# Performance work log

Hardware: AMD Instinct MI355X
Metric: run time of the kernel (lower is better)

Reference implementation:

```python
import jax, jax.numpy as jnp
import numpy as np

RADIUS = 0.15   # group_args['radius']
NSAMPLE = 32    # group_args['nsample']
EPS = 1e-5      # BatchNorm eps


def ball_query(p, radius, k):
    # p: [B,N,3]; returns neighbor indices [B,N,K] (first K points within radius,
    # padded with the first hit -- PointNet++ ball-query semantics; self is always a hit)
    N = p.shape[1]
    d2 = jnp.sum((p[:, :, None, :] - p[:, None, :, :]) ** 2, axis=-1)  # [B,N,N]
    idx = jnp.where(d2 < radius * radius,
                    jnp.arange(N, dtype=jnp.int32)[None, None, :], N)
    idx = jnp.sort(idx, axis=-1)[..., :k]
    return jnp.where(idx == N, idx[..., :1], idx)


def conv_bn_relu(x, W, gamma, beta, mean, var):
    # 1x1 conv2d (pointwise over [N,K]) + eval-mode BN2d + ReLU
    x = jnp.einsum('oc,bcnk->bonk', W, x)
    scale = (gamma / jnp.sqrt(var + EPS))[None, :, None, None]
    shift = (beta - mean * gamma / jnp.sqrt(var + EPS))[None, :, None, None]
    return jax.nn.relu(x * scale + shift)


def setup_inputs() -> dict:
    key = jax.random.key(0)
    ks = jax.random.split(key, 4)
    B, N, C = 2, 8192, 64
    C1, C2 = 128, 128
    Cin = C + 3  # CHANNEL_MAP['dp_fj']
    return {
        'p': jax.random.uniform(ks[0], (B, N, 3), jnp.float32),
        'f': jax.random.normal(ks[1], (B, C, N), jnp.float32),
        'W1': jax.random.normal(ks[2], (C1, Cin), jnp.float32) / np.float32(np.sqrt(Cin)),
        'gamma1': jnp.ones((C1,), jnp.float32),
        'beta1': jnp.zeros((C1,), jnp.float32),
        'mean1': jnp.zeros((C1,), jnp.float32),
        'var1': jnp.ones((C1,), jnp.float32),
        'W2': jax.random.normal(ks[3], (C2, C1), jnp.float32) / np.float32(np.sqrt(C1)),
        'gamma2': jnp.ones((C2,), jnp.float32),
        'beta2': jnp.zeros((C2,), jnp.float32),
        'mean2': jnp.zeros((C2,), jnp.float32),
        'var2': jnp.ones((C2,), jnp.float32),
    }


def reference(p, f, W1, gamma1, beta1, mean1, var1, W2, gamma2, beta2, mean2, var2):
    # p: [B,N,3], f: [B,C,N]
    idx = ball_query(p, RADIUS, NSAMPLE)                                   # [B,N,K]
    gp = jnp.take_along_axis(p[:, None, :, :], idx[:, :, :, None], axis=2)  # [B,N,K,3]
    dp = jnp.transpose(gp - p[:, :, None, :], (0, 3, 1, 2))                 # [B,3,N,K]
    fj = jnp.take_along_axis(f[:, :, None, :], idx[:, None, :, :], axis=3)  # [B,C,N,K]
    x = jnp.concatenate([dp, fj], axis=1)                                   # dp_fj: [B,3+C,N,K]
    x = conv_bn_relu(x, W1, gamma1, beta1, mean1, var1)
    x = conv_bn_relu(x, W2, gamma2, beta2, mean2, var2)
    return jnp.max(x, axis=-1)                                              # [B,C2,N]
```

## Files before the change

kernel.cpp:

```cpp
#include <hip/hip_runtime.h>
#include <math.h>

#define NSAMPLE 32
constexpr int B_ = 2, N_ = 8192, C_ = 64, C1_ = 128, C2_ = 128, CIN_ = 67;
constexpr int KP = 96;
constexpr int XPAD = 104;
constexpr int HPAD = 136;
constexpr float BQ_R2 = 0.15f * 0.15f;
constexpr float EPS_ = 1e-5f;

typedef __attribute__((ext_vector_type(8))) short bf16x8;
typedef __attribute__((ext_vector_type(4))) short short4v;
typedef __attribute__((ext_vector_type(4))) float f32x4;

__device__ __forceinline__ short f2bf(float x) {
    union { float f; unsigned u; } v; v.f = x;
    return (short)((v.u + 0x7FFFu + ((v.u >> 16) & 1u)) >> 16);
}

constexpr int TBLK = (B_ * N_) / 256;
constexpr int QBLK0 = TBLK + 1;

__global__ __launch_bounds__(256) void prep_query_kernel(
    const float* __restrict__ p, const float* __restrict__ f,
    short* __restrict__ fT, int* __restrict__ idx,
    const float* __restrict__ W1,
    const float* __restrict__ g1, const float* __restrict__ b1,
    const float* __restrict__ m1, const float* __restrict__ v1,
    const float* __restrict__ W2,
    const float* __restrict__ g2, const float* __restrict__ b2,
    const float* __restrict__ m2, const float* __restrict__ v2,
    short* __restrict__ W1p, short* __restrict__ W2p, float* __restrict__ bn)
{
    int blk = blockIdx.x;
    if (blk < TBLK) {
        int g = blk * 256 + threadIdx.x;
        int b = g >> 13, n = g & (N_ - 1);
        const float* fb = f + (size_t)b * C_ * N_ + n;
        short* row = fT + (size_t)g * C_;
        #pragma unroll
        for (int c0 = 0; c0 < C_; c0 += 8) {
            bf16x8 v;
            #pragma unroll
            for (int c = 0; c < 8; ++c) v[c] = f2bf(fb[(size_t)(c0 + c) * N_]);
            *(bf16x8*)&row[c0] = v;
        }
    } else if (blk == TBLK) {
        if (threadIdx.x >= 128) return;
        int t = threadIdx.x;
        short* r1 = W1p + t * KP;
        #pragma unroll
        for (int k = 0; k < 3; ++k) r1[k] = f2bf(W1[t * CIN_ + k]);
        #pragma unroll
        for (int k = 3; k < 8; ++k) r1[k] = 0;
        for (int c = 0; c < 64; ++c) r1[8 + c] = f2bf(W1[t * CIN_ + 3 + c]);
        #pragma unroll
        for (int k = 72; k < KP; ++k) r1[k] = 0;
        short* r2 = W2p + t * C1_;
        for (int c = 0; c < C1_; ++c) r2[c] = f2bf(W2[t * C1_ + c]);
        float s1 = g1[t] * rsqrtf(v1[t] + EPS_);
        bn[t] = s1;            bn[128 + t] = b1[t] - m1[t] * s1;
        float s2 = g2[t] * rsqrtf(v2[t] + EPS_);
        bn[256 + t] = s2;      bn[384 + t] = b2[t] - m2[t] * s2;
    } else {
        int wid = (blk - QBLK0) * 4 + (threadIdx.x >> 6);
        int lane = threadIdx.x & 63;
        int b = wid >> 13, n = wid & (N_ - 1);
        const float* pb = p + (size_t)b * N_ * 3;
        float qx = pb[3 * n], qy = pb[3 * n + 1], qz = pb[3 * n + 2];
        int* out = idx + (size_t)wid * NSAMPLE;
        int cnt = 0, first = -1;
        for (int j0 = 0; j0 < N_; j0 += 256) {
            int jb = j0 + 4 * lane;
            const float* q = pb + 3 * jb;
            f32x4 u0 = *(const f32x4*)(q);
            f32x4 u1 = *(const f32x4*)(q + 4);
            f32x4 u2 = *(const f32x4*)(q + 8);
            float x0 = u0[0], y0 = u0[1], z0 = u0[2];
            float x1 = u0[3], y1 = u1[0], z1 = u1[1];
            float x2 = u1[2], y2 = u1[3], z2 = u2[0];
            float x3 = u2[1], y3 = u2[2], z3 = u2[3];
            float dx, dy, dz, d2;
            dx = __fadd_rn(x0, -qx); dy = __fadd_rn(y0, -qy); dz = __fadd_rn(z0, -qz);
            d2 = __fadd_rn(__fadd_rn(__fmul_rn(dx, dx), __fmul_rn(dy, dy)), __fmul_rn(dz, dz));
            bool h0 = d2 < BQ_R2;
            dx = __fadd_rn(x1, -qx); dy = __fadd_rn(y1, -qy); dz = __fadd_rn(z1, -qz);
            d2 = __fadd_rn(__fadd_rn(__fmul_rn(dx, dx), __fmul_rn(dy, dy)), __fmul_rn(dz, dz));
            bool h1 = d2 < BQ_R2;
            dx = __fadd_rn(x2, -qx); dy = __fadd_rn(y2, -qy); dz = __fadd_rn(z2, -qz);
            d2 = __fadd_rn(__fadd_rn(__fmul_rn(dx, dx), __fmul_rn(dy, dy)), __fmul_rn(dz, dz));
            bool h2 = d2 < BQ_R2;
            dx = __fadd_rn(x3, -qx); dy = __fadd_rn(y3, -qy); dz = __fadd_rn(z3, -qz);
            d2 = __fadd_rn(__fadd_rn(__fmul_rn(dx, dx), __fmul_rn(dy, dy)), __fmul_rn(dz, dz));
            bool h3 = d2 < BQ_R2;
            unsigned long long m0 = __ballot(h0), m1 = __ballot(h1);
            unsigned long long m2 = __ballot(h2), m3 = __ballot(h3);
            unsigned long long below = (1ull << lane) - 1ull;
            int pos = cnt + __popcll(m0 & below) + __popcll(m1 & below)
                          + __popcll(m2 & below) + __popcll(m3 & below);
            if (h0) { if (pos < NSAMPLE) out[pos] = jb;     ++pos; }
            if (h1) { if (pos < NSAMPLE) out[pos] = jb + 1; ++pos; }
            if (h2) { if (pos < NSAMPLE) out[pos] = jb + 2; ++pos; }
            if (h3) { if (pos < NSAMPLE) out[pos] = jb + 3; ++pos; }
            if (first < 0) {
                int fj = 0x7fffffff;
                if (m0) fj = min(fj, 4 * (__ffsll((long long)m0) - 1));
                if (m1) fj = min(fj, 4 * (__ffsll((long long)m1) - 1) + 1);
                if (m2) fj = min(fj, 4 * (__ffsll((long long)m2) - 1) + 2);
                if (m3) fj = min(fj, 4 * (__ffsll((long long)m3) - 1) + 3);
                if (fj != 0x7fffffff) first = j0 + fj;
            }
            cnt += __popcll(m0) + __popcll(m1) + __popcll(m2) + __popcll(m3);
            if (cnt >= NSAMPLE) break;
        }
        for (int k2 = cnt + lane; k2 < NSAMPLE; k2 += 64) out[k2] = first;
    }
}

__global__ __launch_bounds__(256) void fused_mfma_kernel(
    const float* __restrict__ p, const int* __restrict__ idx,
    const short* __restrict__ fT, const short* __restrict__ W1p,
    const short* __restrict__ W2p, const float* __restrict__ bn,
    float* __restrict__ out)
{
    __shared__ short smem[128 * HPAD];
    __shared__ float sBN[4][128];
    __shared__ int sidx[128];

    int tid = threadIdx.x;
    int bk = blockIdx.x;
    bk = (bk & 7) * 512 + (bk >> 3);
    int b = bk >> 11;
    int n0 = (bk & 2047) * 4;
    int lane = tid & 63, w = tid >> 6;
    int lr = lane & 15, lq = lane >> 4;

    if (tid < 128) {
        sBN[0][tid] = bn[tid];       sBN[1][tid] = bn[128 + tid];
        sBN[2][tid] = bn[256 + tid]; sBN[3][tid] = bn[384 + tid];
        sidx[tid] = idx[((size_t)((b << 13) + n0)) * NSAMPLE + tid];
    }
    __syncthreads();

    const float* pb = p + (size_t)b * N_ * 3;
    #pragma unroll
    for (int pass = 0; pass < 4; ++pass) {
        int col = pass * 32 + (tid >> 3);
        int part = tid & 7;
        int j = sidx[col];
        *(bf16x8*)&smem[col * XPAD + 8 + part * 8] =
            *(const bf16x8*)&fT[((size_t)(b << 13) + j) * C_ + part * 8];
        if (part == 0) {
            int n = n0 + (col >> 5);
            bf16x8 v = {0, 0, 0, 0, 0, 0, 0, 0};
            v[0] = f2bf(__fadd_rn(pb[3 * j],     -pb[3 * n]));
            v[1] = f2bf(__fadd_rn(pb[3 * j + 1], -pb[3 * n + 1]));
            v[2] = f2bf(__fadd_rn(pb[3 * j + 2], -pb[3 * n + 2]));
            *(bf16x8*)&smem[col * XPAD] = v;
        } else if (part <= 3) {
            bf16x8 z = {0, 0, 0, 0, 0, 0, 0, 0};
            *(bf16x8*)&smem[col * XPAD + 72 + (part - 1) * 8] = z;
        }
    }
    __syncthreads();

    int wr = (w & 1) * 64;
    int wc = (w >> 1) * 64;

    f32x4 acc[4][4];
    #pragma unroll
    for (int m = 0; m < 4; ++m)
        #pragma unroll
        for (int nt = 0; nt < 4; ++nt) acc[m][nt] = (f32x4){0.f, 0.f, 0.f, 0.f};
    #pragma unroll
    for (int ks = 0; ks < 3; ++ks) {
        bf16x8 a[4];
        #pragma unroll
        for (int m = 0; m < 4; ++m)
            a[m] = *(const bf16x8*)&W1p[(wr + m * 16 + lr) * KP + ks * 32 + lq * 8];
        #pragma unroll
        for (int nt = 0; nt < 4; ++nt) {
            bf16x8 bf = *(const bf16x8*)&smem[(wc + nt * 16 + lr) * XPAD + ks * 32 + lq * 8];
            #pragma unroll
            for (int m = 0; m < 4; ++m)
                acc[m][nt] = __builtin_amdgcn_mfma_f32_16x16x32_bf16(a[m], bf, acc[m][nt], 0, 0, 0);
        }
    }
    __syncthreads();

    #pragma unroll
    for (int m = 0; m < 4; ++m) {
        int rb = wr + m * 16 + lq * 4;
        float s0 = sBN[0][rb], s1 = sBN[0][rb + 1], s2 = sBN[0][rb + 2], s3 = sBN[0][rb + 3];
        float h0 = sBN[1][rb], h1 = sBN[1][rb + 1], h2 = sBN[1][rb + 2], h3 = sBN[1][rb + 3];
        #pragma unroll
        for (int nt = 0; nt < 4; ++nt) {
            int col = wc + nt * 16 + lr;
            short4v hv;
            hv[0] = f2bf(fmaxf(fmaf(acc[m][nt][0], s0, h0), 0.f));
            hv[1] = f2bf(fmaxf(fmaf(acc[m][nt][1], s1, h1), 0.f));
            hv[2] = f2bf(fmaxf(fmaf(acc[m][nt][2], s2, h2), 0.f));
            hv[3] = f2bf(fmaxf(fmaf(acc[m][nt][3], s3, h3), 0.f));
            *(short4v*)&smem[col * HPAD + rb] = hv;
        }
    }
    __syncthreads();

    f32x4 acc2[4][4];
    #pragma unroll
    for (int m = 0; m < 4; ++m)
        #pragma unroll
        for (int nt = 0; nt < 4; ++nt) acc2[m][nt] = (f32x4){0.f, 0.f, 0.f, 0.f};
    #pragma unroll
    for (int ks = 0; ks < 4; ++ks) {
        bf16x8 a[4];
        #pragma unroll
        for (int m = 0; m < 4; ++m)
            a[m] = *(const bf16x8*)&W2p[(wr + m * 16 + lr) * C1_ + ks * 32 + lq * 8];
        #pragma unroll
        for (int nt = 0; nt < 4; ++nt) {
            bf16x8 bf = *(const bf16x8*)&smem[(wc + nt * 16 + lr) * HPAD + ks * 32 + lq * 8];
            #pragma unroll
            for (int m = 0; m < 4; ++m)
                acc2[m][nt] = __builtin_amdgcn_mfma_f32_16x16x32_bf16(a[m], bf, acc2[m][nt], 0, 0, 0);
        }
    }

    #pragma unroll
    for (int m = 0; m < 4; ++m) {
        int rb = wr + m * 16 + lq * 4;
        float s0 = sBN[2][rb], s1 = sBN[2][rb + 1], s2 = sBN[2][rb + 2], s3 = sBN[2][rb + 3];
        float h0 = sBN[3][rb], h1 = sBN[3][rb + 1], h2 = sBN[3][rb + 2], h3 = sBN[3][rb + 3];
        #pragma unroll
        for (int lp = 0; lp < 2; ++lp) {
            int n = n0 + (w >> 1) * 2 + lp;
            float v0 = fmaxf(fmaf(acc2[m][2 * lp][0], s0, h0), fmaf(acc2[m][2 * lp + 1][0], s0, h0));
            float v1 = fmaxf(fmaf(acc2[m][2 * lp][1], s1, h1), fmaf(acc2[m][2 * lp + 1][1], s1, h1));
            float v2 = fmaxf(fmaf(acc2[m][2 * lp][2], s2, h2), fmaf(acc2[m][2 * lp + 1][2], s2, h2));
            float v3 = fmaxf(fmaf(acc2[m][2 * lp][3], s3, h3), fmaf(acc2[m][2 * lp + 1][3], s3, h3));
            #pragma unroll
            for (int st = 1; st <= 8; st <<= 1) {
                v0 = fmaxf(v0, __shfl_xor(v0, st, 64));
                v1 = fmaxf(v1, __shfl_xor(v1, st, 64));
                v2 = fmaxf(v2, __shfl_xor(v2, st, 64));
                v3 = fmaxf(v3, __shfl_xor(v3, st, 64));
            }
            if (lr == 0) {
                out[((size_t)(b * C2_ + rb))     * N_ + n] = fmaxf(v0, 0.f);
                out[((size_t)(b * C2_ + rb + 1)) * N_ + n] = fmaxf(v1, 0.f);
                out[((size_t)(b * C2_ + rb + 2)) * N_ + n] = fmaxf(v2, 0.f);
                out[((size_t)(b * C2_ + rb + 3)) * N_ + n] = fmaxf(v3, 0.f);
            }
        }
    }
}

extern "C" void kernel_launch(void* const* d_in, const int* in_sizes, int n_in,
                              void* d_out, int out_size, void* d_ws, size_t ws_size,
                              hipStream_t stream) {
    const float* p   = (const float*)d_in[0];
    const float* f   = (const float*)d_in[1];
    const float* W1  = (const float*)d_in[2];
    const float* g1  = (const float*)d_in[3];
    const float* bb1 = (const float*)d_in[4];
    const float* m1  = (const float*)d_in[5];
    const float* v1  = (const float*)d_in[6];
    const float* W2  = (const float*)d_in[7];
    const float* g2  = (const float*)d_in[8];
    const float* bb2 = (const float*)d_in[9];
    const float* m2  = (const float*)d_in[10];
    const float* v2  = (const float*)d_in[11];
    float* out = (float*)d_out;

    char* ws = (char*)d_ws;
    int*   idxbuf = (int*)ws;
    short* fT  = (short*)(ws + (2 << 20));
    short* W1p = (short*)(ws + (4 << 20));
    short* W2p = (short*)(ws + (4 << 20) + 0x6000);
    float* bnv = (float*)(ws + (4 << 20) + 0xE000);

    prep_query_kernel<<<QBLK0 + (B_ * N_) / 4, 256, 0, stream>>>(
        p, f, fT, idxbuf, W1, g1, bb1, m1, v1, W2, g2, bb2, m2, v2,
        W1p, W2p, bnv);
    fused_mfma_kernel<<<(B_ * N_) / 4, 256, 0, stream>>>(
        p, idxbuf, fT, W1p, W2p, bnv, out);
}
```

Baseline: 181.3 us.

## Precompute relative offsets in ball query and swizzle LDS tiles in fused MLP

The ball-query stage now writes bf16 relative offsets (dp) alongside neighbor indices, so the fused kernel no longer gathers point coordinates. The fused kernel drops row padding in LDS in favor of an XOR swizzle, preloads W1 fragments into registers, and reads BN parameters straight from global memory. Packed bf16 conversion instructions replace manual rounding, and the query loop prefetches the next chunk of points. This trades extra workspace writes and register pressure for fewer scattered global loads and LDS bank conflicts.

After: 205.0 us. 13.1% more time.

```diff
diff --git a/kernel.cpp b/kernel.cpp
--- a/kernel.cpp
+++ b/kernel.cpp
@@ -4,26 +4,29 @@
 #define NSAMPLE 32
 constexpr int B_ = 2, N_ = 8192, C_ = 64, C1_ = 128, C2_ = 128, CIN_ = 67;
 constexpr int KP = 96;
-constexpr int XPAD = 104;
-constexpr int HPAD = 136;
 constexpr float BQ_R2 = 0.15f * 0.15f;
 constexpr float EPS_ = 1e-5f;
 
 typedef __attribute__((ext_vector_type(8))) short bf16x8;
-typedef __attribute__((ext_vector_type(4))) short short4v;
 typedef __attribute__((ext_vector_type(4))) float f32x4;
+typedef unsigned long long ull;
 
 __device__ __forceinline__ short f2bf(float x) {
     union { float f; unsigned u; } v; v.f = x;
     return (short)((v.u + 0x7FFFu + ((v.u >> 16) & 1u)) >> 16);
 }
+__device__ __forceinline__ unsigned cvt_pk_bf16(float a, float b) {
+    unsigned r;
+    asm("v_cvt_pk_bf16_f32 %0, %1, %2" : "=v"(r) : "v"(a), "v"(b));
+    return r;
+}
 
 constexpr int TBLK = (B_ * N_) / 256;
 constexpr int QBLK0 = TBLK + 1;
 
 __global__ __launch_bounds__(256) void prep_query_kernel(
     const float* __restrict__ p, const float* __restrict__ f,
-    short* __restrict__ fT, int* __restrict__ idx,
+    short* __restrict__ fT, int* __restrict__ idx, short* __restrict__ dpq,
     const float* __restrict__ W1,
     const float* __restrict__ g1, const float* __restrict__ b1,
     const float* __restrict__ m1, const float* __restrict__ v1,
@@ -40,10 +43,14 @@
         short* row = fT + (size_t)g * C_;
         #pragma unroll
         for (int c0 = 0; c0 < C_; c0 += 8) {
-            bf16x8 v;
-            #pragma unroll
-            for (int c = 0; c < 8; ++c) v[c] = f2bf(fb[(size_t)(c0 + c) * N_]);
-            *(bf16x8*)&row[c0] = v;
+            float t0 = fb[(size_t)(c0 + 0) * N_], t1 = fb[(size_t)(c0 + 1) * N_];
+            float t2 = fb[(size_t)(c0 + 2) * N_], t3 = fb[(size_t)(c0 + 3) * N_];
+            float t4 = fb[(size_t)(c0 + 4) * N_], t5 = fb[(size_t)(c0 + 5) * N_];
+            float t6 = fb[(size_t)(c0 + 6) * N_], t7 = fb[(size_t)(c0 + 7) * N_];
+            union { bf16x8 v; unsigned u[4]; } uu;
+            uu.u[0] = cvt_pk_bf16(t0, t1); uu.u[1] = cvt_pk_bf16(t2, t3);
+            uu.u[2] = cvt_pk_bf16(t4, t5); uu.u[3] = cvt_pk_bf16(t6, t7);
+            *(bf16x8*)&row[c0] = uu.v;
         }
     } else if (blk == TBLK) {
         if (threadIdx.x >= 128) return;
@@ -69,39 +76,49 @@
         const float* pb = p + (size_t)b * N_ * 3;
         float qx = pb[3 * n], qy = pb[3 * n + 1], qz = pb[3 * n + 2];
         int* out = idx + (size_t)wid * NSAMPLE;
+        short* dq = dpq + (size_t)wid * NSAMPLE * 4;
         int cnt = 0, first = -1;
+        const float* q0 = pb + 12 * lane;
+        f32x4 u0 = *(const f32x4*)(q0);
+        f32x4 u1 = *(const f32x4*)(q0 + 4);
+        f32x4 u2 = *(const f32x4*)(q0 + 8);
         for (int j0 = 0; j0 < N_; j0 += 256) {
+            int jn = (j0 + 256 < N_) ? j0 + 256 : 0;
+            const float* qn = pb + 3 * (jn + 4 * lane);
+            f32x4 w0 = *(const f32x4*)(qn);
+            f32x4 w1 = *(const f32x4*)(qn + 4);
+            f32x4 w2 = *(const f32x4*)(qn + 8);
             int jb = j0 + 4 * lane;
-            const float* q = pb + 3 * jb;
-            f32x4 u0 = *(const f32x4*)(q);
-            f32x4 u1 = *(const f32x4*)(q + 4);
-            f32x4 u2 = *(const f32x4*)(q + 8);
             float x0 = u0[0], y0 = u0[1], z0 = u0[2];
             float x1 = u0[3], y1 = u1[0], z1 = u1[1];
             float x2 = u1[2], y2 = u1[3], z2 = u2[0];
             float x3 = u2[1], y3 = u2[2], z3 = u2[3];
-            float dx, dy, dz, d2;
-            dx = __fadd_rn(x0, -qx); dy = __fadd_rn(y0, -qy); dz = __fadd_rn(z0, -qz);
-            d2 = __fadd_rn(__fadd_rn(__fmul_rn(dx, dx), __fmul_rn(dy, dy)), __fmul_rn(dz, dz));
-            bool h0 = d2 < BQ_R2;
-            dx = __fadd_rn(x1, -qx); dy = __fadd_rn(y1, -qy); dz = __fadd_rn(z1, -qz);
-            d2 = __fadd_rn(__fadd_rn(__fmul_rn(dx, dx), __fmul_rn(dy, dy)), __fmul_rn(dz, dz));
-            bool h1 = d2 < BQ_R2;
-            dx = __fadd_rn(x2, -qx); dy = __fadd_rn(y2, -qy); dz = __fadd_rn(z2, -qz);
-            d2 = __fadd_rn(__fadd_rn(__fmul_rn(dx, dx), __fmul_rn(dy, dy)), __fmul_rn(dz, dz));
-            bool h2 = d2 < BQ_R2;
-            dx = __fadd_rn(x3, -qx); dy = __fadd_rn(y3, -qy); dz = __fadd_rn(z3, -qz);
-            d2 = __fadd_rn(__fadd_rn(__fmul_rn(dx, dx), __fmul_rn(dy, dy)), __fmul_rn(dz, dz));
-            bool h3 = d2 < BQ_R2;
-            unsigned long long m0 = __ballot(h0), m1 = __ballot(h1);
-            unsigned long long m2 = __ballot(h2), m3 = __ballot(h3);
-            unsigned long long below = (1ull << lane) - 1ull;
+            float ax0 = __fadd_rn(x0, -qx), ay0 = __fadd_rn(y0, -qy), az0 = __fadd_rn(z0, -qz);
+            float ax1 = __fadd_rn(x1, -qx), ay1 = __fadd_rn(y1, -qy), az1 = __fadd_rn(z1, -qz);
+            float ax2 = __fadd_rn(x2, -qx), ay2 = __fadd_rn(y2, -qy), az2 = __fadd_rn(z2, -qz);
+            float ax3 = __fadd_rn(x3, -qx), ay3 = __fadd_rn(y3, -qy), az3 = __fadd_rn(z3, -qz);
+            float d20 = __fadd_rn(__fadd_rn(__fmul_rn(ax0, ax0), __fmul_rn(ay0, ay0)), __fmul_rn(az0, az0));
+            float d21 = __fadd_rn(__fadd_rn(__fmul_rn(ax1, ax1), __fmul_rn(ay1, ay1)), __fmul_rn(az1, az1));
+            float d22 = __fadd_rn(__fadd_rn(__fmul_rn(ax2, ax2), __fmul_rn(ay2, ay2)), __fmul_rn(az2, az2));
+            float d23 = __fadd_rn(__fadd_rn(__fmul_rn(ax3, ax3), __fmul_rn(ay3, ay3)), __fmul_rn(az3, az3));
+            bool h0 = d20 < BQ_R2, h1 = d21 < BQ_R2, h2 = d22 < BQ_R2, h3 = d23 < BQ_R2;
+            ull m0 = __ballot(h0), m1 = __ballot(h1);
+            ull m2 = __ballot(h2), m3 = __ballot(h3);
+            ull below = (1ull << lane) - 1ull;
             int pos = cnt + __popcll(m0 & below) + __popcll(m1 & below)
                           + __popcll(m2 & below) + __popcll(m3 & below);
-            if (h0) { if (pos < NSAMPLE) out[pos] = jb;     ++pos; }
-            if (h1) { if (pos < NSAMPLE) out[pos] = jb + 1; ++pos; }
-            if (h2) { if (pos < NSAMPLE) out[pos] = jb + 2; ++pos; }
-            if (h3) { if (pos < NSAMPLE) out[pos] = jb + 3; ++pos; }
+            if (h0) { if (pos < NSAMPLE) { out[pos] = jb;
+                ull dv = (ull)cvt_pk_bf16(ax0, ay0) | ((ull)cvt_pk_bf16(az0, 0.f) << 32);
+                *(ull*)&dq[pos * 4] = dv; } ++pos; }
+            if (h1) { if (pos < NSAMPLE) { out[pos] = jb + 1;
+                ull dv = (ull)cvt_pk_bf16(ax1, ay1) | ((ull)cvt_pk_bf16(az1, 0.f) << 32);
+                *(ull*)&dq[pos * 4] = dv; } ++pos; }
+            if (h2) { if (pos < NSAMPLE) { out[pos] = jb + 2;
+                ull dv = (ull)cvt_pk_bf16(ax2, ay2) | ((ull)cvt_pk_bf16(az2, 0.f) << 32);
+                *(ull*)&dq[pos * 4] = dv; } ++pos; }
+            if (h3) { if (pos < NSAMPLE) { out[pos] = jb + 3;
+                ull dv = (ull)cvt_pk_bf16(ax3, ay3) | ((ull)cvt_pk_bf16(az3, 0.f) << 32);
+                *(ull*)&dq[pos * 4] = dv; } ++pos; }
             if (first < 0) {
                 int fj = 0x7fffffff;
                 if (m0) fj = min(fj, 4 * (__ffsll((long long)m0) - 1));
@@ -111,20 +128,27 @@
                 if (fj != 0x7fffffff) first = j0 + fj;
             }
             cnt += __popcll(m0) + __popcll(m1) + __popcll(m2) + __popcll(m3);
+            u0 = w0; u1 = w1; u2 = w2;
             if (cnt >= NSAMPLE) break;
         }
-        for (int k2 = cnt + lane; k2 < NSAMPLE; k2 += 64) out[k2] = first;
+        float fx = __fadd_rn(pb[3 * first],     -qx);
+        float fy = __fadd_rn(pb[3 * first + 1], -qy);
+        float fz = __fadd_rn(pb[3 * first + 2], -qz);
+        ull fdv = (ull)cvt_pk_bf16(fx, fy) | ((ull)cvt_pk_bf16(fz, 0.f) << 32);
+        for (int k2 = cnt + lane; k2 < NSAMPLE; k2 += 64) {
+            out[k2] = first;
+            *(ull*)&dq[k2 * 4] = fdv;
+        }
     }
 }
 
 __global__ __launch_bounds__(256) void fused_mfma_kernel(
-    const float* __restrict__ p, const int* __restrict__ idx,
+    const int* __restrict__ idx, const short* __restrict__ dpq,
     const short* __restrict__ fT, const short* __restrict__ W1p,
     const short* __restrict__ W2p, const float* __restrict__ bn,
     float* __restrict__ out)
 {
-    __shared__ short smem[128 * HPAD];
-    __shared__ float sBN[4][128];
+    __shared__ short smem[128 * 128];
     __shared__ int sidx[128];
 
     int tid = threadIdx.x;
@@ -134,74 +158,72 @@
     int n0 = (bk & 2047) * 4;
     int lane = tid & 63, w = tid >> 6;
     int lr = lane & 15, lq = lane >> 4;
-
-    if (tid < 128) {
-        sBN[0][tid] = bn[tid];       sBN[1][tid] = bn[128 + tid];
-        sBN[2][tid] = bn[256 + tid]; sBN[3][tid] = bn[384 + tid];
+    int wr = (w & 1) * 64;
+    int wc = (w >> 1) * 64;
+
+    if (tid < 128)
         sidx[tid] = idx[((size_t)((b << 13) + n0)) * NSAMPLE + tid];
-    }
+
+    bf16x8 a1[3][4];
+    #pragma unroll
+    for (int ks = 0; ks < 3; ++ks)
+        #pragma unroll
+        for (int m = 0; m < 4; ++m)
+            a1[ks][m] = *(const bf16x8*)&W1p[(wr + m * 16 + lr) * KP + ks * 32 + lq * 8];
     __syncthreads();
 
-    const float* pb = p + (size_t)b * N_ * 3;
     #pragma unroll
     for (int pass = 0; pass < 4; ++pass) {
         int col = pass * 32 + (tid >> 3);
         int part = tid & 7;
+        int c7 = col & 7;
         int j = sidx[col];
-        *(bf16x8*)&smem[col * XPAD + 8 + part * 8] =
+        *(bf16x8*)&smem[col * 128 + (((1 + part) ^ c7) << 3)] =
             *(const bf16x8*)&fT[((size_t)(b << 13) + j) * C_ + part * 8];
         if (part == 0) {
-            int n = n0 + (col >> 5);
-            bf16x8 v = {0, 0, 0, 0, 0, 0, 0, 0};
-            v[0] = f2bf(__fadd_rn(pb[3 * j],     -pb[3 * n]));
-            v[1] = f2bf(__fadd_rn(pb[3 * j + 1], -pb[3 * n + 1]));
-            v[2] = f2bf(__fadd_rn(pb[3 * j + 2], -pb[3 * n + 2]));
-            *(bf16x8*)&smem[col * XPAD] = v;
+            ull dv = *(const ull*)&dpq[((size_t)((b << 13) + n0 + pass) * NSAMPLE
+                                        + (col & 31)) * 4];
+            union { bf16x8 v; ull q[2]; } uu;
+            uu.q[0] = dv; uu.q[1] = 0;
+            *(bf16x8*)&smem[col * 128 + ((0 ^ c7) << 3)] = uu.v;
         } else if (part <= 3) {
             bf16x8 z = {0, 0, 0, 0, 0, 0, 0, 0};
-            *(bf16x8*)&smem[col * XPAD + 72 + (part - 1) * 8] = z;
+            *(bf16x8*)&smem[col * 128 + (((8 + part) ^ c7) << 3)] = z;
         }
     }
     __syncthreads();
 
-    int wr = (w & 1) * 64;
-    int wc = (w >> 1) * 64;
-
     f32x4 acc[4][4];
     #pragma unroll
     for (int m = 0; m < 4; ++m)
         #pragma unroll
         for (int nt = 0; nt < 4; ++nt) acc[m][nt] = (f32x4){0.f, 0.f, 0.f, 0.f};
     #pragma unroll
-    for (int ks = 0; ks < 3; ++ks) {
-        bf16x8 a[4];
-        #pragma unroll
-        for (int m = 0; m < 4; ++m)
-            a[m] = *(const bf16x8*)&W1p[(wr + m * 16 + lr) * KP + ks * 32 + lq * 8];
+    for (int ks = 0; ks < 3; ++ks)
         #pragma unroll
         for (int nt = 0; nt < 4; ++nt) {
-            bf16x8 bf = *(const bf16x8*)&smem[(wc + nt * 16 + lr) * XPAD + ks * 32 + lq * 8];
+            int col = wc + nt * 16 + lr;
+            bf16x8 bf = *(const bf16x8*)&smem[col * 128 + ((((ks << 2) + lq) ^ (col & 7)) << 3)];
             #pragma unroll
             for (int m = 0; m < 4; ++m)
-                acc[m][nt] = __builtin_amdgcn_mfma_f32_16x16x32_bf16(a[m], bf, acc[m][nt], 0, 0, 0);
-        }
-    }
+                acc[m][nt] = __builtin_amdgcn_mfma_f32_16x16x32_bf16(a1[ks][m], bf, acc[m][nt], 0, 0, 0);
+        }
     __syncthreads();
 
     #pragma unroll
     for (int m = 0; m < 4; ++m) {
         int rb = wr + m * 16 + lq * 4;
-        float s0 = sBN[0][rb], s1 = sBN[0][rb + 1], s2 = sBN[0][rb + 2], s3 = sBN[0][rb + 3];
-        float h0 = sBN[1][rb], h1 = sBN[1][rb + 1], h2 = sBN[1][rb + 2], h3 = sBN[1][rb + 3];
+        f32x4 sc = *(const f32x4*)&bn[rb];
+        f32x4 sh = *(const f32x4*)&bn[128 + rb];
         #pragma unroll
         for (int nt = 0; nt < 4; ++nt) {
             int col = wc + nt * 16 + lr;
-            short4v hv;
-            hv[0] = f2bf(fmaxf(fmaf(acc[m][nt][0], s0, h0), 0.f));
-            hv[1] = f2bf(fmaxf(fmaf(acc[m][nt][1], s1, h1), 0.f));
-            hv[2] = f2bf(fmaxf(fmaf(acc[m][nt][2], s2, h2), 0.f));
-            hv[3] = f2bf(fmaxf(fmaf(acc[m][nt][3], s3, h3), 0.f));
-            *(short4v*)&smem[col * HPAD + rb] = hv;
+            float y0 = fmaxf(fmaf(acc[m][nt][0], sc[0], sh[0]), 0.f);
+            float y1 = fmaxf(fmaf(acc[m][nt][1], sc[1], sh[1]), 0.f);
+            float y2 = fmaxf(fmaf(acc[m][nt][2], sc[2], sh[2]), 0.f);
+            float y3 = fmaxf(fmaf(acc[m][nt][3], sc[3], sh[3]), 0.f);
+            ull dv = (ull)cvt_pk_bf16(y0, y1) | ((ull)cvt_pk_bf16(y2, y3) << 32);
+            *(ull*)&smem[col * 128 + ((((rb >> 3) ^ (col & 7)) << 3) | (rb & 7))] = dv;
         }
     }
     __syncthreads();
@@ -213,31 +235,32 @@
         for (int nt = 0; nt < 4; ++nt) acc2[m][nt] = (f32x4){0.f, 0.f, 0.f, 0.f};
     #pragma unroll
     for (int ks = 0; ks < 4; ++ks) {
-        bf16x8 a[4];
+        bf16x8 a2[4];
         #pragma unroll
         for (int m = 0; m < 4; ++m)
-            a[m] = *(const bf16x8*)&W2p[(wr + m * 16 + lr) * C1_ + ks * 32 + lq * 8];
+            a2[m] = *(const bf16x8*)&W2p[(wr + m * 16 + lr) * C1_ + ks * 32 + lq * 8];
         #pragma unroll
         for (int nt = 0; nt < 4; ++nt) {
-            bf16x8 bf = *(const bf16x8*)&smem[(wc + nt * 16 + lr) * HPAD + ks * 32 + lq * 8];
+            int col = wc + nt * 16 + lr;
+            bf16x8 bf = *(const bf16x8*)&smem[col * 128 + ((((ks << 2) + lq) ^ (col & 7)) << 3)];
             #pragma unroll
             for (int m = 0; m < 4; ++m)
-                acc2[m][nt] = __builtin_amdgcn_mfma_f32_16x16x32_bf16(a[m], bf, acc2[m][nt], 0, 0, 0);
+                acc2[m][nt] = __builtin_amdgcn_mfma_f32_16x16x32_bf16(a2[m], bf, acc2[m][nt], 0, 0, 0);
         }
     }
 
     #pragma unroll
     for (int m = 0; m < 4; ++m) {
         int rb = wr + m * 16 + lq * 4;
-        float s0 = sBN[2][rb], s1 = sBN[2][rb + 1], s2 = sBN[2][rb + 2], s3 = sBN[2][rb + 3];
-        float h0 = sBN[3][rb], h1 = sBN[3][rb + 1], h2 = sBN[3][rb + 2], h3 = sBN[3][rb + 3];
+        f32x4 sc = *(const f32x4*)&bn[256 + rb];
+        f32x4 sh = *(const f32x4*)&bn[384 + rb];
         #pragma unroll
         for (int lp = 0; lp < 2; ++lp) {
             int n = n0 + (w >> 1) * 2 + lp;
-            float v0 = fmaxf(fmaf(acc2[m][2 * lp][0], s0, h0), fmaf(acc2[m][2 * lp + 1][0], s0, h0));
-            float v1 = fmaxf(fmaf(acc2[m][2 * lp][1], s1, h1), fmaf(acc2[m][2 * lp + 1][1], s1, h1));
-            float v2 = fmaxf(fmaf(acc2[m][2 * lp][2], s2, h2), fmaf(acc2[m][2 * lp + 1][2], s2, h2));
-            float v3 = fmaxf(fmaf(acc2[m][2 * lp][3], s3, h3), fmaf(acc2[m][2 * lp + 1][3], s3, h3));
+            float v0 = fmaxf(fmaf(acc2[m][2 * lp][0], sc[0], sh[0]), fmaf(acc2[m][2 * lp + 1][0], sc[0], sh[0]));
+            float v1 = fmaxf(fmaf(acc2[m][2 * lp][1], sc[1], sh[1]), fmaf(acc2[m][2 * lp + 1][1], sc[1], sh[1]));
+            float v2 = fmaxf(fmaf(acc2[m][2 * lp][2], sc[2], sh[2]), fmaf(acc2[m][2 * lp + 1][2], sc[2], sh[2]));
+            float v3 = fmaxf(fmaf(acc2[m][2 * lp][3], sc[3], sh[3]), fmaf(acc2[m][2 * lp + 1][3], sc[3], sh[3]));
             #pragma unroll
             for (int st = 1; st <= 8; st <<= 1) {
                 v0 = fmaxf(v0, __shfl_xor(v0, st, 64));
@@ -274,14 +297,15 @@
 
     char* ws = (char*)d_ws;
     int*   idxbuf = (int*)ws;
-    short* fT  = (short*)(ws + (2 << 20));
-    short* W1p = (short*)(ws + (4 << 20));
-    short* W2p = (short*)(ws + (4 << 20) + 0x6000);
-    float* bnv = (float*)(ws + (4 << 20) + 0xE000);
+    short* dpq = (short*)(ws + (2 << 20));
+    short* fT  = (short*)(ws + (6 << 20));
+    short* W1p = (short*)(ws + (8 << 20));
+    short* W2p = (short*)(ws + (8 << 20) + 0x6000);
+    float* bnv = (float*)(ws + (8 << 20) + 0xE000);
 
     prep_query_kernel<<<QBLK0 + (B_ * N_) / 4, 256, 0, stream>>>(
-        p, f, fT, idxbuf, W1, g1, bb1, m1, v1, W2, g2, bb2, m2, v2,
+        p, f, fT, idxbuf, dpq, W1, g1, bb1, m1, v1, W2, g2, bb2, m2, v2,
         W1p, W2p, bnv);
     fused_mfma_kernel<<<(B_ * N_) / 4, 256, 0, stream>>>(
-        p, idxbuf, fT, W1p, W2p, bnv, out);
-}
+        idxbuf, dpq, fT, W1p, W2p, bnv, out);
+}
```

## Replace brute-force ball query with uniform-grid spatial hashing

Applied to the files above, without the earlier changes.

Bins points into a 6x6x6 uniform grid with counting sort (count, prefix, scatter kernels), then each query wave scans only the 27 neighboring cells. Hits go into a per-wave shared bitmap so the first 32 hits come out in ascending index order, matching the reference ordering. This targets the linear scan over all N points per query, which dominates when 32 hits appear late. In exchange it adds a memset, three small extra kernel launches and shared-memory atomics. It also assumes coordinates lie in [0,1).

Measured after the change: 217.8 us. 1.2x slower.

```diff
diff --git a/kernel.cpp b/kernel.cpp
--- a/kernel.cpp
+++ b/kernel.cpp
@@ -8,22 +8,30 @@
 constexpr int HPAD = 136;
 constexpr float BQ_R2 = 0.15f * 0.15f;
 constexpr float EPS_ = 1e-5f;
+constexpr int NCELL = 216;
 
 typedef __attribute__((ext_vector_type(8))) short bf16x8;
 typedef __attribute__((ext_vector_type(4))) short short4v;
 typedef __attribute__((ext_vector_type(4))) float f32x4;
+typedef unsigned long long ull;
 
 __device__ __forceinline__ short f2bf(float x) {
     union { float f; unsigned u; } v; v.f = x;
     return (short)((v.u + 0x7FFFu + ((v.u >> 16) & 1u)) >> 16);
 }
+__device__ __forceinline__ int cell_id(float x, float y, float z) {
+    int cx = min((int)(x * 6.0f), 5);
+    int cy = min((int)(y * 6.0f), 5);
+    int cz = min((int)(z * 6.0f), 5);
+    return (cz * 6 + cy) * 6 + cx;
+}
 
 constexpr int TBLK = (B_ * N_) / 256;
-constexpr int QBLK0 = TBLK + 1;
-
-__global__ __launch_bounds__(256) void prep_query_kernel(
+constexpr int CBLK0 = TBLK + 1;
+
+__global__ __launch_bounds__(256) void prep_kernel(
     const float* __restrict__ p, const float* __restrict__ f,
-    short* __restrict__ fT, int* __restrict__ idx,
+    short* __restrict__ fT, int* __restrict__ counts,
     const float* __restrict__ W1,
     const float* __restrict__ g1, const float* __restrict__ b1,
     const float* __restrict__ m1, const float* __restrict__ v1,
@@ -63,57 +71,136 @@
         float s2 = g2[t] * rsqrtf(v2[t] + EPS_);
         bn[256 + t] = s2;      bn[384 + t] = b2[t] - m2[t] * s2;
     } else {
-        int wid = (blk - QBLK0) * 4 + (threadIdx.x >> 6);
-        int lane = threadIdx.x & 63;
-        int b = wid >> 13, n = wid & (N_ - 1);
-        const float* pb = p + (size_t)b * N_ * 3;
-        float qx = pb[3 * n], qy = pb[3 * n + 1], qz = pb[3 * n + 2];
-        int* out = idx + (size_t)wid * NSAMPLE;
-        int cnt = 0, first = -1;
-        for (int j0 = 0; j0 < N_; j0 += 256) {
-            int jb = j0 + 4 * lane;
-            const float* q = pb + 3 * jb;
-            f32x4 u0 = *(const f32x4*)(q);
-            f32x4 u1 = *(const f32x4*)(q + 4);
-            f32x4 u2 = *(const f32x4*)(q + 8);
-            float x0 = u0[0], y0 = u0[1], z0 = u0[2];
-            float x1 = u0[3], y1 = u1[0], z1 = u1[1];
-            float x2 = u1[2], y2 = u1[3], z2 = u2[0];
-            float x3 = u2[1], y3 = u2[2], z3 = u2[3];
-            float dx, dy, dz, d2;
-            dx = __fadd_rn(x0, -qx); dy = __fadd_rn(y0, -qy); dz = __fadd_rn(z0, -qz);
-            d2 = __fadd_rn(__fadd_rn(__fmul_rn(dx, dx), __fmul_rn(dy, dy)), __fmul_rn(dz, dz));
-            bool h0 = d2 < BQ_R2;
-            dx = __fadd_rn(x1, -qx); dy = __fadd_rn(y1, -qy); dz = __fadd_rn(z1, -qz);
-            d2 = __fadd_rn(__fadd_rn(__fmul_rn(dx, dx), __fmul_rn(dy, dy)), __fmul_rn(dz, dz));
-            bool h1 = d2 < BQ_R2;
-            dx = __fadd_rn(x2, -qx); dy = __fadd_rn(y2, -qy); dz = __fadd_rn(z2, -qz);
-            d2 = __fadd_rn(__fadd_rn(__fmul_rn(dx, dx), __fmul_rn(dy, dy)), __fmul_rn(dz, dz));
-            bool h2 = d2 < BQ_R2;
-            dx = __fadd_rn(x3, -qx); dy = __fadd_rn(y3, -qy); dz = __fadd_rn(z3, -qz);
-            d2 = __fadd_rn(__fadd_rn(__fmul_rn(dx, dx), __fmul_rn(dy, dy)), __fmul_rn(dz, dz));
-            bool h3 = d2 < BQ_R2;
-            unsigned long long m0 = __ballot(h0), m1 = __ballot(h1);
-            unsigned long long m2 = __ballot(h2), m3 = __ballot(h3);
-            unsigned long long below = (1ull << lane) - 1ull;
-            int pos = cnt + __popcll(m0 & below) + __popcll(m1 & below)
-                          + __popcll(m2 & below) + __popcll(m3 & below);
-            if (h0) { if (pos < NSAMPLE) out[pos] = jb;     ++pos; }
-            if (h1) { if (pos < NSAMPLE) out[pos] = jb + 1; ++pos; }
-            if (h2) { if (pos < NSAMPLE) out[pos] = jb + 2; ++pos; }
-            if (h3) { if (pos < NSAMPLE) out[pos] = jb + 3; ++pos; }
-            if (first < 0) {
-                int fj = 0x7fffffff;
-                if (m0) fj = min(fj, 4 * (__ffsll((long long)m0) - 1));
-                if (m1) fj = min(fj, 4 * (__ffsll((long long)m1) - 1) + 1);
-                if (m2) fj = min(fj, 4 * (__ffsll((long long)m2) - 1) + 2);
-                if (m3) fj = min(fj, 4 * (__ffsll((long long)m3) - 1) + 3);
-                if (fj != 0x7fffffff) first = j0 + fj;
+        int g = (blk - CBLK0) * 256 + threadIdx.x;
+        int b = g >> 13, n = g & (N_ - 1);
+        const float* q = p + (size_t)b * N_ * 3 + 3 * n;
+        int c = cell_id(q[0], q[1], q[2]);
+        atomicAdd(&counts[b * 256 + c], 1);
+    }
+}
+
+__global__ __launch_bounds__(128) void prefix_kernel(
+    const int* __restrict__ counts, int* __restrict__ starts)
+{
+    int w = threadIdx.x >> 6, lane = threadIdx.x & 63;
+    const int* cnt = counts + w * 256;
+    int* st = starts + w * 256;
+    int off = 0;
+    #pragma unroll
+    for (int ch = 0; ch < 4; ++ch) {
+        int i = ch * 64 + lane;
+        int v = (i < NCELL) ? cnt[i] : 0;
+        int incl = v;
+        #pragma unroll
+        for (int d = 1; d < 64; d <<= 1) {
+            int t = __shfl_up(incl, d, 64);
+            if (lane >= d) incl += t;
+        }
+        if (i <= NCELL) st[i] = off + incl - v;
+        off += __shfl(incl, 63, 64);
+    }
+}
+
+__global__ __launch_bounds__(256) void scatter_kernel(
+    const float* __restrict__ p, const int* __restrict__ starts,
+    int* __restrict__ cursors, int* __restrict__ lists)
+{
+    int g = blockIdx.x * 256 + threadIdx.x;
+    int b = g >> 13, n = g & (N_ - 1);
+    const float* q = p + (size_t)b * N_ * 3 + 3 * n;
+    int c = cell_id(q[0], q[1], q[2]);
+    int slot = starts[b * 256 + c] + atomicAdd(&cursors[b * 256 + c], 1);
+    lists[(b << 13) + slot] = n;
+}
+
+__global__ __launch_bounds__(256) void grid_query_kernel(
+    const float* __restrict__ p, const int* __restrict__ starts,
+    const int* __restrict__ lists, int* __restrict__ idx)
+{
+    __shared__ ull bitmap[4][128];
+    int tid = threadIdx.x, lane = tid & 63, w = tid >> 6;
+    int wid = blockIdx.x * 4 + w;
+    int b = wid >> 13, n = wid & (N_ - 1);
+    const float* pb = p + (size_t)b * N_ * 3;
+    const int* st = starts + b * 256;
+    const int* ls = lists + (b << 13);
+    float qx = pb[3 * n], qy = pb[3 * n + 1], qz = pb[3 * n + 2];
+
+    #pragma unroll
+    for (int i = lane; i < 128; i += 64) bitmap[w][i] = 0;
+
+    int cx = min((int)(qx * 6.0f), 5);
+    int cy = min((int)(qy * 6.0f), 5);
+    int cz = min((int)(qz * 6.0f), 5);
+    int x0 = max(cx - 1, 0), x1 = min(cx + 1, 5);
+
+    int segBase[9], segLen[9], total = 0;
+    #pragma unroll
+    for (int s = 0; s < 9; ++s) {
+        int zz = cz - 1 + s / 3, yy = cy - 1 + s % 3;
+        bool ok = (zz >= 0 && zz < 6 && yy >= 0 && yy < 6);
+        int zc = min(max(zz, 0), 5), yc = min(max(yy, 0), 5);
+        int row = (zc * 6 + yc) * 6;
+        int s0 = st[row + x0], s1 = st[row + x1 + 1];
+        segBase[s] = s0;
+        segLen[s] = ok ? (s1 - s0) : 0;
+        total += segLen[s];
+    }
+
+    for (int o0 = 0; o0 < total; o0 += 64) {
+        int o = o0 + lane;
+        if (o < total) {
+            int rem = o, addr = -1;
+            #pragma unroll
+            for (int s = 0; s < 9; ++s) {
+                if (rem >= 0 && rem < segLen[s] && addr < 0) addr = segBase[s] + rem;
+                rem -= segLen[s];
             }
-            cnt += __popcll(m0) + __popcll(m1) + __popcll(m2) + __popcll(m3);
-            if (cnt >= NSAMPLE) break;
-        }
-        for (int k2 = cnt + lane; k2 < NSAMPLE; k2 += 64) out[k2] = first;
+            int j = ls[addr];
+            float dx = __fadd_rn(pb[3 * j],     -qx);
+            float dy = __fadd_rn(pb[3 * j + 1], -qy);
+            float dz = __fadd_rn(pb[3 * j + 2], -qz);
+            float d2 = __fadd_rn(__fadd_rn(__fmul_rn(dx, dx), __fmul_rn(dy, dy)),
+                                 __fmul_rn(dz, dz));
+            if (d2 < BQ_R2)
+                atomicOr(&bitmap[w][j >> 6], 1ull << (j & 63));
+        }
+    }
+    __threadfence_block();
+
+    ull w0 = bitmap[w][2 * lane], w1 = bitmap[w][2 * lane + 1];
+    int c = __popcll(w0) + __popcll(w1);
+    int incl = c;
+    #pragma unroll
+    for (int d = 1; d < 64; d <<= 1) {
+        int t = __shfl_up(incl, d, 64);
+        if (lane >= d) incl += t;
+    }
+    int pref = incl - c;
+    int total_hits = __shfl(incl, 63, 64);
+    int* out = idx + (size_t)wid * NSAMPLE;
+
+    int rank = pref;
+    ull ww = w0;
+    int basebit = lane * 128;
+    while (ww && rank < NSAMPLE) {
+        int bpos = __builtin_ctzll(ww);
+        out[rank] = basebit + bpos;
+        ++rank; ww &= ww - 1;
+    }
+    ww = w1; basebit += 64;
+    while (ww && rank < NSAMPLE) {
+        int bpos = __builtin_ctzll(ww);
+        out[rank] = basebit + bpos;
+        ++rank; ww &= ww - 1;
+    }
+
+    if (total_hits < NSAMPLE) {
+        ull m = __ballot(c > 0);
+        int l0 = __ffsll((long long)m) - 1;
+        int fb_local = w0 ? __builtin_ctzll(w0) : 64 + __builtin_ctzll(w1);
+        int first = __shfl(fb_local, l0, 64) + l0 * 128;
+        for (int k2 = total_hits + lane; k2 < NSAMPLE; k2 += 64) out[k2] = first;
     }
 }
 
@@ -278,10 +365,19 @@
     short* W1p = (short*)(ws + (4 << 20));
     short* W2p = (short*)(ws + (4 << 20) + 0x6000);
     float* bnv = (float*)(ws + (4 << 20) + 0xE000);
-
-    prep_query_kernel<<<QBLK0 + (B_ * N_) / 4, 256, 0, stream>>>(
-        p, f, fT, idxbuf, W1, g1, bb1, m1, v1, W2, g2, bb2, m2, v2,
+    char*  gm  = ws + (4 << 20) + 0x10000;
+    int* counts  = (int*)gm;
+    int* cursors = (int*)(gm + 0x800);
+    int* starts  = (int*)(gm + 0x1000);
+    int* lists   = (int*)(gm + 0x2000);
+
+    hipMemsetAsync(gm, 0, 0x1000, stream);
+    prep_kernel<<<CBLK0 + 64, 256, 0, stream>>>(
+        p, f, fT, counts, W1, g1, bb1, m1, v1, W2, g2, bb2, m2, v2,
         W1p, W2p, bnv);
+    prefix_kernel<<<1, 128, 0, stream>>>(counts, starts);
+    scatter_kernel<<<64, 256, 0, stream>>>(p, starts, cursors, lists);
+    grid_query_kernel<<<(B_ * N_) / 4, 256, 0, stream>>>(p, starts, lists, idxbuf);
     fused_mfma_kernel<<<(B_ * N_) / 4, 256, 0, stream>>>(
         p, idxbuf, fT, W1p, W2p, bnv, out);
 }
```
